# Kernel tuning notes

Measured on AMD Instinct MI355X. Metric: run time of the kernel, lower is better.

Reference implementation:

```python
import jax, jax.numpy as jnp
import numpy as np

H = 20  # hidden size (hardcoded in the torch module)

def setup_inputs() -> dict:
    key = jax.random.key(0)
    ks = jax.random.split(key, 7)
    s = 0.1  # keep activations in a sane range for tanh/sigmoid
    return {
        "x":     jax.random.normal(ks[0], (8192, 512, 12), dtype=jnp.float32),
        "w_ih":  jax.random.normal(ks[1], (4 * H, 12), dtype=jnp.float32) * s,
        "w_hh":  jax.random.normal(ks[2], (4 * H, H), dtype=jnp.float32) * s,
        "b_ih":  jax.random.normal(ks[3], (4 * H,), dtype=jnp.float32) * s,
        "b_hh":  jax.random.normal(ks[4], (4 * H,), dtype=jnp.float32) * s,
        "w_out": jax.random.normal(ks[5], (10, H), dtype=jnp.float32) * s,
        "b_out": jax.random.normal(ks[6], (10,), dtype=jnp.float32) * s,
    }

def reference(x, w_ih, w_hh, b_ih, b_hh, w_out, b_out):
    # x: [B, T, I]. Single-layer LSTM (PyTorch gate order i,f,g,o), zero init state,
    # then Linear on the last hidden state.
    B, T, _ = x.shape
    # Precompute input projections for all timesteps: [T, B, 4H]
    x_proj = jnp.einsum('bti,gi->tbg', x, w_ih) + (b_ih + b_hh)

    def step(carry, xt):
        h, c = carry                      # each [B, H]
        gates = xt + h @ w_hh.T           # [B, 4H]
        i, f, g, o = jnp.split(gates, 4, axis=-1)
        i = jax.nn.sigmoid(i)
        f = jax.nn.sigmoid(f)
        g = jnp.tanh(g)
        o = jax.nn.sigmoid(o)
        c = f * c + i * g
        h = o * jnp.tanh(c)
        return (h, c), None

    h0 = jnp.zeros((B, H), dtype=x.dtype)
    c0 = jnp.zeros((B, H), dtype=x.dtype)
    (h_last, _), _ = jax.lax.scan(step, (h0, c0), x_proj)
    # out = Linear(h_T): r_out[:, -1, :] == h_n for a single-layer LSTM
    return h_last @ w_out.T + b_out
```

## Files before the change

### kernel.cpp

```cpp
#include <hip/hip_runtime.h>

typedef _Float16 f16;
typedef f16 f16x8 __attribute__((ext_vector_type(8)));
typedef float f32x4 __attribute__((ext_vector_type(4)));

#define T_STEPS 512
#define INPUT   12
#define HID     20
#define G4      80
#define KDIM    32
#define BW      4
#define WPB     4
#define BLOCK   (WPB * 64)

__device__ __forceinline__ void lds_fence() {
    asm volatile("s_waitcnt lgkmcnt(0)" ::: "memory");
}

__device__ __forceinline__ float fast_sigmoid(float x) {
    float e = __builtin_amdgcn_exp2f(-1.4426950408889634f * x);
    return __builtin_amdgcn_rcpf(1.0f + e);
}
__device__ __forceinline__ float fast_tanh(float x) {
    float e = __builtin_amdgcn_exp2f(2.8853900817779268f * x);
    return 1.0f - 2.0f * __builtin_amdgcn_rcpf(1.0f + e);
}

__global__ __launch_bounds__(BLOCK) void lstm_kernel(
    const float* __restrict__ x,
    const float* __restrict__ w_ih,
    const float* __restrict__ w_hh,
    const float* __restrict__ b_ih,
    const float* __restrict__ b_hh,
    const float* __restrict__ w_out,
    const float* __restrict__ b_out,
    float* __restrict__ out)
{
    __shared__ __align__(16) f16   Wc[G4][KDIM];
    __shared__ __align__(16) f16   Abuf_s[WPB][16][KDIM];
    __shared__ __align__(16) float gbuf_s[WPB][G4][BW];

    const int tid = threadIdx.x;

    for (int i = tid; i < G4 * KDIM; i += BLOCK) {
        int g = i >> 5, k = i & 31;
        float v = (k < INPUT) ? w_ih[g * INPUT + k] : w_hh[g * HID + (k - INPUT)];
        Wc[g][k] = (f16)v;
    }
    __syncthreads();

    const int wid  = tid >> 6;
    const int lane = tid & 63;
    const int c    = lane & 15;
    const int q    = lane >> 4;

    f16   (*Abuf)[KDIM] = Abuf_s[wid];
    float (*gbuf)[BW]   = gbuf_s[wid];

    f16x8 bfrag[5];
#pragma unroll
    for (int nt = 0; nt < 5; ++nt)
        bfrag[nt] = *(const f16x8*)&Wc[nt * 16 + c][q * 8];

    const int u1 = c,            b1 = q;
    const int u2 = 16 + (lane & 3), b2 = lane >> 2;
    float bias1[4], bias2[4];
#pragma unroll
    for (int g = 0; g < 4; ++g) {
        bias1[g] = b_ih[g * HID + u1] + b_hh[g * HID + u1];
        bias2[g] = b_ih[g * HID + u2] + b_hh[g * HID + u2];
    }

    {
        f16x8 z = {};
        *(f16x8*)&(((f16*)Abuf)[lane * 8]) = z;
    }
    lds_fence();

    const int wave_global = blockIdx.x * WPB + wid;
    const int b0 = wave_global * BW;

    const int  xb    = lane / 12;
    const int  xi    = lane % 12;
    const bool xload = lane < 48;
    const float* xptr = x + (size_t)(b0 + xb) * (T_STEPS * INPUT) + xi;

    if (xload) Abuf[xb][xi] = (f16)xptr[0];
    float xv = 0.f;
    if (xload) xv = xptr[INPUT];
    lds_fence();

    float c1 = 0.f, c2 = 0.f;

#pragma unroll 1
    for (int t = 0; t < T_STEPS; ++t) {
        f16x8 afrag = *(const f16x8*)&Abuf[c][q * 8];
        lds_fence();

        if (xload) Abuf[xb][xi] = (f16)xv;
        int tn = t + 2; if (tn > T_STEPS - 1) tn = T_STEPS - 1;
        if (xload) xv = xptr[(size_t)tn * INPUT];

        f32x4 acc[5];
#pragma unroll
        for (int nt = 0; nt < 5; ++nt) {
            f32x4 z = {};
            acc[nt] = __builtin_amdgcn_mfma_f32_16x16x32_f16(afrag, bfrag[nt], z, 0, 0, 0);
        }

        if (lane < 16) {
#pragma unroll
            for (int nt = 0; nt < 5; ++nt)
                *(f32x4*)&gbuf[nt * 16 + c][0] = acc[nt];
        }
        lds_fence();

        {
            float gi = gbuf[u1][b1]           + bias1[0];
            float gf = gbuf[HID + u1][b1]     + bias1[1];
            float gg = gbuf[2 * HID + u1][b1] + bias1[2];
            float go = gbuf[3 * HID + u1][b1] + bias1[3];
            float ig = fast_sigmoid(gi), fg = fast_sigmoid(gf);
            float gt = fast_tanh(gg),    og = fast_sigmoid(go);
            c1 = fg * c1 + ig * gt;
            float h = og * fast_tanh(c1);
            Abuf[b1][INPUT + u1] = (f16)h;
        }
        if (lane < 16) {
            float gi = gbuf[u2][b2]           + bias2[0];
            float gf = gbuf[HID + u2][b2]     + bias2[1];
            float gg = gbuf[2 * HID + u2][b2] + bias2[2];
            float go = gbuf[3 * HID + u2][b2] + bias2[3];
            float ig = fast_sigmoid(gi), fg = fast_sigmoid(gf);
            float gt = fast_tanh(gg),    og = fast_sigmoid(go);
            c2 = fg * c2 + ig * gt;
            float h = og * fast_tanh(c2);
            Abuf[b2][INPUT + u2] = (f16)h;
        }
        lds_fence();
    }

    if (lane < 40) {
        int ob = lane / 10, oo = lane % 10;
        float s = b_out[oo];
#pragma unroll
        for (int u = 0; u < HID; ++u)
            s += w_out[oo * HID + u] * (float)Abuf[ob][INPUT + u];
        out[(size_t)(b0 + ob) * 10 + oo] = s;
    }
}

extern "C" void kernel_launch(void* const* d_in, const int* in_sizes, int n_in,
                              void* d_out, int out_size, void* d_ws, size_t ws_size,
                              hipStream_t stream) {
    const float* x     = (const float*)d_in[0];
    const float* w_ih  = (const float*)d_in[1];
    const float* w_hh  = (const float*)d_in[2];
    const float* b_ih  = (const float*)d_in[3];
    const float* b_hh  = (const float*)d_in[4];
    const float* w_out = (const float*)d_in[5];
    const float* b_out = (const float*)d_in[6];
    float* out = (float*)d_out;

    const int total_waves = 8192 / BW;
    const int blocks = total_waves / WPB;
    hipLaunchKernelGGL(lstm_kernel, dim3(blocks), dim3(BLOCK), 0, stream,
                       x, w_ih, w_hh, b_ih, b_hh, w_out, b_out, out);
}
```

Measured before the change: 528.2 us.

## Split LSTM gate columns across waves with 16-sequence blocks and double-buffered state

```diff
diff --git a/kernel.cpp b/kernel.cpp
--- a/kernel.cpp
+++ b/kernel.cpp
@@ -7,21 +7,23 @@
 #define T_STEPS 512
 #define INPUT   12
 #define HID     20
-#define G4      80
 #define KDIM    32
-#define BW      4
-#define WPB     4
+#define BATCH   16
+#define WPB     5
 #define BLOCK   (WPB * 64)
 
-__device__ __forceinline__ void lds_fence() {
+static __device__ __forceinline__ void wave_lds_fence() {
     asm volatile("s_waitcnt lgkmcnt(0)" ::: "memory");
 }
+static __device__ __forceinline__ void block_barrier() {
+    asm volatile("s_waitcnt lgkmcnt(0)\n\ts_barrier" ::: "memory");
+}
 
-__device__ __forceinline__ float fast_sigmoid(float x) {
+static __device__ __forceinline__ float fast_sigmoid(float x) {
     float e = __builtin_amdgcn_exp2f(-1.4426950408889634f * x);
     return __builtin_amdgcn_rcpf(1.0f + e);
 }
-__device__ __forceinline__ float fast_tanh(float x) {
+static __device__ __forceinline__ float fast_tanh(float x) {
     float e = __builtin_amdgcn_exp2f(2.8853900817779268f * x);
     return 1.0f - 2.0f * __builtin_amdgcn_rcpf(1.0f + e);
 }
@@ -36,117 +38,91 @@
     const float* __restrict__ b_out,
     float* __restrict__ out)
 {
-    __shared__ __align__(16) f16   Wc[G4][KDIM];
-    __shared__ __align__(16) f16   Abuf_s[WPB][16][KDIM];
-    __shared__ __align__(16) float gbuf_s[WPB][G4][BW];
+    __shared__ __align__(16) f16   Wc[80][KDIM];
+    __shared__ __align__(16) f16   Abuf[2][BATCH][KDIM];
+    __shared__ __align__(16) float wgbuf[WPB][16][16];
 
-    const int tid = threadIdx.x;
+    const int tid  = threadIdx.x;
+    const int wid  = tid >> 6;
+    const int lane = tid & 63;
 
-    for (int i = tid; i < G4 * KDIM; i += BLOCK) {
-        int g = i >> 5, k = i & 31;
-        float v = (k < INPUT) ? w_ih[g * INPUT + k] : w_hh[g * HID + (k - INPUT)];
-        Wc[g][k] = (f16)v;
+    for (int i = tid; i < 80 * KDIM; i += BLOCK) {
+        int n = i >> 5, k = i & 31;
+        int w = n >> 4, c = n & 15;
+        int u = 4 * w + (c >> 2);
+        int g = c & 3;
+        int row = g * HID + u;
+        float v = (k < INPUT) ? w_ih[row * INPUT + k] : w_hh[row * HID + (k - INPUT)];
+        Wc[n][k] = (f16)v;
+    }
+
+    const int arow = lane & 15;
+    const int aq   = lane >> 4;
+    const int j  = lane & 3;
+    const int uu = (lane >> 2) & 3;
+    const int b  = 4 * aq + j;
+    const int u  = 4 * wid + uu;
+
+    float bias0 = b_ih[0 * HID + u] + b_hh[0 * HID + u];
+    float bias1 = b_ih[1 * HID + u] + b_hh[1 * HID + u];
+    float bias2 = b_ih[2 * HID + u] + b_hh[2 * HID + u];
+    float bias3 = b_ih[3 * HID + u] + b_hh[3 * HID + u];
+
+    Abuf[0][b][INPUT + u] = (f16)0.f;
+
+    const bool xload = (wid < 4) && (lane < 48);
+    const int  xb    = 4 * wid + lane / 12;
+    const int  xi    = lane % 12;
+    const float* xptr = x + (size_t)(blockIdx.x * BATCH + xb) * (T_STEPS * INPUT) + xi;
+
+    float xv = 0.f;
+    if (xload) {
+        Abuf[0][xb][xi] = (f16)xptr[0];
+        xv = xptr[INPUT];
     }
     __syncthreads();
 
-    const int wid  = tid >> 6;
-    const int lane = tid & 63;
-    const int c    = lane & 15;
-    const int q    = lane >> 4;
+    f16x8 bfrag = *(const f16x8*)&Wc[16 * wid + arow][aq * 8];
 
-    f16   (*Abuf)[KDIM] = Abuf_s[wid];
-    float (*gbuf)[BW]   = gbuf_s[wid];
-
-    f16x8 bfrag[5];
-#pragma unroll
-    for (int nt = 0; nt < 5; ++nt)
-        bfrag[nt] = *(const f16x8*)&Wc[nt * 16 + c][q * 8];
-
-    const int u1 = c,            b1 = q;
-    const int u2 = 16 + (lane & 3), b2 = lane >> 2;
-    float bias1[4], bias2[4];
-#pragma unroll
-    for (int g = 0; g < 4; ++g) {
-        bias1[g] = b_ih[g * HID + u1] + b_hh[g * HID + u1];
-        bias2[g] = b_ih[g * HID + u2] + b_hh[g * HID + u2];
-    }
-
-    {
-        f16x8 z = {};
-        *(f16x8*)&(((f16*)Abuf)[lane * 8]) = z;
-    }
-    lds_fence();
-
-    const int wave_global = blockIdx.x * WPB + wid;
-    const int b0 = wave_global * BW;
-
-    const int  xb    = lane / 12;
-    const int  xi    = lane % 12;
-    const bool xload = lane < 48;
-    const float* xptr = x + (size_t)(b0 + xb) * (T_STEPS * INPUT) + xi;
-
-    if (xload) Abuf[xb][xi] = (f16)xptr[0];
-    float xv = 0.f;
-    if (xload) xv = xptr[INPUT];
-    lds_fence();
-
-    float c1 = 0.f, c2 = 0.f;
+    float cc = 0.f;
+    int p = 0;
 
 #pragma unroll 1
     for (int t = 0; t < T_STEPS; ++t) {
-        f16x8 afrag = *(const f16x8*)&Abuf[c][q * 8];
-        lds_fence();
+        f16x8 afrag = *(const f16x8*)&Abuf[p][arow][aq * 8];
 
-        if (xload) Abuf[xb][xi] = (f16)xv;
+        if (xload) Abuf[p ^ 1][xb][xi] = (f16)xv;
         int tn = t + 2; if (tn > T_STEPS - 1) tn = T_STEPS - 1;
         if (xload) xv = xptr[(size_t)tn * INPUT];
 
-        f32x4 acc[5];
-#pragma unroll
-        for (int nt = 0; nt < 5; ++nt) {
-            f32x4 z = {};
-            acc[nt] = __builtin_amdgcn_mfma_f32_16x16x32_f16(afrag, bfrag[nt], z, 0, 0, 0);
-        }
+        f32x4 z = {};
+        f32x4 acc = __builtin_amdgcn_mfma_f32_16x16x32_f16(afrag, bfrag, z, 0, 0, 0);
 
-        if (lane < 16) {
-#pragma unroll
-            for (int nt = 0; nt < 5; ++nt)
-                *(f32x4*)&gbuf[nt * 16 + c][0] = acc[nt];
-        }
-        lds_fence();
+        *(f32x4*)&wgbuf[wid][arow][4 * aq] = acc;
+        wave_lds_fence();
 
-        {
-            float gi = gbuf[u1][b1]           + bias1[0];
-            float gf = gbuf[HID + u1][b1]     + bias1[1];
-            float gg = gbuf[2 * HID + u1][b1] + bias1[2];
-            float go = gbuf[3 * HID + u1][b1] + bias1[3];
-            float ig = fast_sigmoid(gi), fg = fast_sigmoid(gf);
-            float gt = fast_tanh(gg),    og = fast_sigmoid(go);
-            c1 = fg * c1 + ig * gt;
-            float h = og * fast_tanh(c1);
-            Abuf[b1][INPUT + u1] = (f16)h;
-        }
-        if (lane < 16) {
-            float gi = gbuf[u2][b2]           + bias2[0];
-            float gf = gbuf[HID + u2][b2]     + bias2[1];
-            float gg = gbuf[2 * HID + u2][b2] + bias2[2];
-            float go = gbuf[3 * HID + u2][b2] + bias2[3];
-            float ig = fast_sigmoid(gi), fg = fast_sigmoid(gf);
-            float gt = fast_tanh(gg),    og = fast_sigmoid(go);
-            c2 = fg * c2 + ig * gt;
-            float h = og * fast_tanh(c2);
-            Abuf[b2][INPUT + u2] = (f16)h;
-        }
-        lds_fence();
+        float gi = wgbuf[wid][4 * uu + 0][b] + bias0;
+        float gf = wgbuf[wid][4 * uu + 1][b] + bias1;
+        float gg = wgbuf[wid][4 * uu + 2][b] + bias2;
+        float go = wgbuf[wid][4 * uu + 3][b] + bias3;
+
+        float ig = fast_sigmoid(gi), fg = fast_sigmoid(gf);
+        float gt = fast_tanh(gg),    og = fast_sigmoid(go);
+        cc = fg * cc + ig * gt;
+        float h = og * fast_tanh(cc);
+
+        Abuf[p ^ 1][b][INPUT + u] = (f16)h;
+        block_barrier();
+        p ^= 1;
     }
 
-    if (lane < 40) {
-        int ob = lane / 10, oo = lane % 10;
+    if (tid < BATCH * 10) {
+        int ob = tid / 10, oo = tid % 10;
         float s = b_out[oo];
 #pragma unroll
-        for (int u = 0; u < HID; ++u)
-            s += w_out[oo * HID + u] * (float)Abuf[ob][INPUT + u];
-        out[(size_t)(b0 + ob) * 10 + oo] = s;
+        for (int u2 = 0; u2 < HID; ++u2)
+            s += w_out[oo * HID + u2] * (float)Abuf[0][ob][INPUT + u2];
+        out[(size_t)(blockIdx.x * BATCH + ob) * 10 + oo] = s;
     }
 }
 
@@ -162,8 +138,7 @@
     const float* b_out = (const float*)d_in[6];
     float* out = (float*)d_out;
 
-    const int total_waves = 8192 / BW;
-    const int blocks = total_waves / WPB;
+    const int blocks = 8192 / BATCH;
     hipLaunchKernelGGL(lstm_kernel, dim3(blocks), dim3(BLOCK), 0, stream,
                        x, w_ih, w_hh, b_ih, b_hh, w_out, b_out, out);
 }
```

After: 468.6 us. 11.3% less time.
